# Kernel optimization log

Hardware: AMD Instinct MI355X
Metric: run time of the kernel (lower is better)

The kernel has to match this reference:

```python
import jax, jax.numpy as jnp
import numpy as np

B = 1_048_576
NUM_USERS = 6041
NUM_MOVIES = 3953
EMB_DIM = 32
NUM_GENRES = 18
HIDDEN = [64, 32, 16]
WIDE_DIM = NUM_USERS + NUM_MOVIES + 3 + NUM_GENRES  # gender, age, occupation scalars
DEEP_IN = 2 * EMB_DIM + 3 + NUM_GENRES              # = 85


def setup_inputs() -> dict:
    key = jax.random.key(0)
    ks = jax.random.split(key, 20)
    inp = {
        "user_ids": jax.random.randint(ks[0], (B,), 0, NUM_USERS),
        "movie_ids": jax.random.randint(ks[1], (B,), 0, NUM_MOVIES),
        "gender": jax.random.uniform(ks[2], (B,), dtype=jnp.float32),
        "age": jax.random.uniform(ks[3], (B,), dtype=jnp.float32),
        "occupation": jax.random.uniform(ks[4], (B,), dtype=jnp.float32),
        "genres": jax.random.uniform(ks[5], (B, NUM_GENRES), dtype=jnp.float32),
        # wide linear (out_features=1): weight vector + scalar bias
        "wide_W": jax.random.normal(ks[6], (WIDE_DIM,), dtype=jnp.float32) * 0.01,
        "wide_b": jnp.zeros((), dtype=jnp.float32),
        # embedding tables
        "user_table": jax.random.normal(ks[7], (NUM_USERS, EMB_DIM), dtype=jnp.float32) * 0.05,
        "movie_table": jax.random.normal(ks[8], (NUM_MOVIES, EMB_DIM), dtype=jnp.float32) * 0.05,
        # deep MLP params (stored as [in, out])
        "W1": jax.random.normal(ks[9], (DEEP_IN, HIDDEN[0]), dtype=jnp.float32) * 0.05,
        "b1": jnp.zeros((HIDDEN[0],), dtype=jnp.float32),
        "W2": jax.random.normal(ks[10], (HIDDEN[0], HIDDEN[1]), dtype=jnp.float32) * 0.05,
        "b2": jnp.zeros((HIDDEN[1],), dtype=jnp.float32),
        "W3": jax.random.normal(ks[11], (HIDDEN[1], HIDDEN[2]), dtype=jnp.float32) * 0.05,
        "b3": jnp.zeros((HIDDEN[2],), dtype=jnp.float32),
        "W4": jax.random.normal(ks[12], (HIDDEN[2], 1), dtype=jnp.float32) * 0.05,
        "b4": jnp.zeros((1,), dtype=jnp.float32),
    }
    return inp


def reference(user_ids, movie_ids, gender, age, occupation, genres,
              wide_W, wide_b, user_table, movie_table,
              W1, b1, W2, b2, W3, b3, W4, b4):
    nu = user_table.shape[0]
    nm = movie_table.shape[0]
    # dense (non-one-hot) part of the wide input: [B, 3 + num_genres]
    rest = jnp.concatenate(
        [gender[:, None], age[:, None], occupation[:, None], genres], axis=1)
    # one_hot @ W  ==  gather of the corresponding weight entries (same math,
    # without materializing the [B, nu+nm+21] one-hot matrix)
    w_user = wide_W[:nu]
    w_movie = wide_W[nu:nu + nm]
    w_rest = wide_W[nu + nm:]
    wide_out = w_user[user_ids] + w_movie[movie_ids] + rest @ w_rest + wide_b  # [B]

    # deep path (dropout is identity at inference)
    u_emb = user_table[user_ids]    # [B, 32]
    m_emb = movie_table[movie_ids]  # [B, 32]
    h = jnp.concatenate([u_emb, m_emb, rest], axis=1)  # [B, 85]
    h = jax.nn.relu(h @ W1 + b1)
    h = jax.nn.relu(h @ W2 + b2)
    h = jax.nn.relu(h @ W3 + b3)
    deep_out = (h @ W4 + b4)[:, 0]  # [B]

    return jax.nn.sigmoid(wide_out + deep_out)  # [B]
```

## Files before the change

kernel.cpp:

```cpp
#include <hip/hip_runtime.h>

#define NUSERS  6041
#define NMOVIES 3953
#define EMB     32
#define NGEN    18
#define H1N     64
#define H2N     32
#define H3N     16

typedef __bf16 bf16_t;
typedef bf16_t bf16x8 __attribute__((ext_vector_type(8)));
typedef float  f32x4  __attribute__((ext_vector_type(4)));
typedef float  f32x8  __attribute__((ext_vector_type(8)));

__device__ __forceinline__ f32x4 mfma16(bf16x8 a, bf16x8 b, f32x4 c) {
    return __builtin_amdgcn_mfma_f32_16x16x32_bf16(a, b, c, 0, 0, 0);
}
__device__ __forceinline__ bf16x8 cvt8(f32x8 v) {
    bf16x8 o;
    #pragma unroll
    for (int i = 0; i < 8; ++i) o[i] = (bf16_t)v[i];
    return o;
}

#define L1STRIDE 68
#define L2STRIDE 36
#define RSTRIDE  28
#define RBUFSZ   (16 * RSTRIDE)

struct Pref {
    float4 u0, u1, m0, m1;
    float  wu, wm;
};

__global__ __launch_bounds__(256)
void wd_fwd_pipe(const int*   __restrict__ user_ids,
                 const int*   __restrict__ movie_ids,
                 const float* __restrict__ gender,
                 const float* __restrict__ age,
                 const float* __restrict__ occupation,
                 const float* __restrict__ genres,
                 const float* __restrict__ wide_W,
                 const float* __restrict__ wide_b,
                 const float* __restrict__ user_table,
                 const float* __restrict__ movie_table,
                 const float* __restrict__ W1,
                 const float* __restrict__ b1,
                 const float* __restrict__ W2,
                 const float* __restrict__ b2,
                 const float* __restrict__ W3,
                 const float* __restrict__ b3,
                 const float* __restrict__ W4,
                 const float* __restrict__ b4,
                 float*       __restrict__ out,
                 int n)
{
    const int lane = threadIdx.x & 63;
    const int wib  = threadIdx.x >> 6;
    const int m    = lane & 15;
    const int quad = lane >> 4;

    __shared__ float lds_rest[4][2 * RBUFSZ];
    __shared__ float lds1[4][16 * L1STRIDE];
    __shared__ float lds2[4][16 * L2STRIDE];
    float* __restrict__ rbase = lds_rest[wib];
    float* __restrict__ L1p   = lds1[wib];
    float* __restrict__ L2p   = lds2[wib];

    for (int k = lane; k < 2 * RBUFSZ; k += 64) rbase[k] = 0.0f;

    bf16x8 B1f[3][4];
    #pragma unroll
    for (int kt = 0; kt < 3; ++kt)
        #pragma unroll
        for (int nt = 0; nt < 4; ++nt) {
            bf16x8 f;
            #pragma unroll
            for (int j = 0; j < 8; ++j) {
                const int k  = kt * 32 + quad * 8 + j;
                const float v = (k < 85) ? W1[k * H1N + nt * 16 + m] : 0.0f;
                f[j] = (bf16_t)v;
            }
            B1f[kt][nt] = f;
        }
    bf16x8 Bwf;
    {
        const float* wr = wide_W + NUSERS + NMOVIES;
        #pragma unroll
        for (int j = 0; j < 8; ++j) {
            const int k = 64 + quad * 8 + j;
            float v = 0.0f;
            if (m == 0) { if (k < 85) v = wr[k - 64]; else if (k == 85) v = 1.0f; }
            Bwf[j] = (bf16_t)v;
        }
    }
    bf16x8 B2f[2][2];
    #pragma unroll
    for (int kt = 0; kt < 2; ++kt)
        #pragma unroll
        for (int nt = 0; nt < 2; ++nt) {
            bf16x8 f;
            #pragma unroll
            for (int j = 0; j < 8; ++j)
                f[j] = (bf16_t)W2[(kt * 32 + quad * 8 + j) * H2N + nt * 16 + m];
            B2f[kt][nt] = f;
        }
    bf16x8 B3f;
    #pragma unroll
    for (int j = 0; j < 8; ++j) B3f[j] = (bf16_t)W3[(quad * 8 + j) * H3N + m];

    float bias1[4], bias2[2];
    #pragma unroll
    for (int nt = 0; nt < 4; ++nt) bias1[nt] = b1[nt * 16 + m];
    #pragma unroll
    for (int nt = 0; nt < 2; ++nt) bias2[nt] = b2[nt * 16 + m];
    const float bias3 = b3[m];
    const float w4v   = W4[m];
    const float b4v   = b4[0];
    const float wb0   = wide_b[0];

    const int ntiles = (n + 15) >> 4;
    const int gwave  = blockIdx.x * 4 + wib;
    const int nwaves = gridDim.x * 4;
    int niter = 0;
    if (gwave < ntiles) niter = (ntiles - gwave + nwaves - 1) / nwaves;
    const long gmax = (long)n * NGEN - 1;

#define LOAD_IDS(tt, U, M) { int rr = (tt) * 16 + m; rr = rr < n ? rr : n - 1; \
                             U = user_ids[rr]; M = movie_ids[rr]; }
#define LOAD_GENRES(tt, G, SC) { \
    const long gb = (long)(tt) * (16 * NGEN); \
    _Pragma("unroll") \
    for (int r = 0; r < 4; ++r) { long idx = gb + lane + r * 64; \
        idx = idx < gmax ? idx : gmax; G[r] = genres[idx]; } \
    { long idx = gb + lane + 256; idx = idx < gmax ? idx : gmax; \
      G[4] = (lane < 32) ? genres[idx] : 0.0f; } \
    { int rr = (tt) * 16 + m; rr = rr < n ? rr : n - 1; \
      const float* sp = (quad == 0) ? gender : (quad == 1) ? age : occupation; \
      SC = (quad < 3) ? sp[rr] : 0.0f; } }
#define WRITE_RBUF(B, G, SC) { \
    float* rb_ = rbase + (B) * RBUFSZ; \
    _Pragma("unroll") \
    for (int r = 0; r < 4; ++r) { int gi = lane + r * 64; int rw = gi / NGEN; \
        int cl = gi - rw * NGEN; rb_[rw * RSTRIDE + 3 + cl] = G[r]; } \
    if (lane < 32) { int gi = lane + 256; int rw = gi / NGEN; int cl = gi - rw * NGEN; \
        rb_[rw * RSTRIDE + 3 + cl] = G[4]; } \
    if (quad < 3) rb_[m * RSTRIDE + quad] = SC; }
#define ISSUE_GATHER(UID, MID, P) { \
    const float4* up_ = (const float4*)(user_table + (size_t)(UID) * EMB + quad * 8); \
    P.u0 = up_[0]; P.u1 = up_[1]; \
    const float4* mp_ = (const float4*)(movie_table + (size_t)(MID) * EMB + quad * 8); \
    P.m0 = mp_[0]; P.m1 = mp_[1]; \
    P.wu = wide_W[UID]; P.wm = wide_W[NUSERS + (MID)]; }

    if (niter > 0) {
        int t_c = gwave;
        int t_n = t_c + nwaves; if (t_n >= ntiles) t_n = t_c;

        int uid_c, mid_c, uid_n, mid_n, uid_n2, mid_n2;
        float gg_c[5], sc_c, gg_n[5], sc_n;
        Pref P_c, P_n;

        LOAD_IDS(t_c, uid_c, mid_c);
        LOAD_GENRES(t_c, gg_c, sc_c);
        ISSUE_GATHER(uid_c, mid_c, P_c);
        LOAD_IDS(t_n, uid_n, mid_n);
        WRITE_RBUF(0, gg_c, sc_c);
        uid_n2 = uid_n; mid_n2 = mid_n;
        int buf = 0;

        for (int i = 0; i < niter; ++i) {
            const float* rb = rbase + buf * RBUFSZ;
            const float4* sA = (const float4*)(rb + m * RSTRIDE + quad * 8);
            float4 a2a = sA[0], a2b = sA[1];

            const bool more = (i + 1 < niter);
            int t_n2 = t_n;
            if (more) {
                LOAD_GENRES(t_n, gg_n, sc_n);
                ISSUE_GATHER(uid_n, mid_n, P_n);
                t_n2 = t_n + nwaves; if (t_n2 >= ntiles) t_n2 = t_n;
                LOAD_IDS(t_n2, uid_n2, mid_n2);
            }

            const int base = t_c << 4;
            f32x8 vf;
            vf[0]=P_c.u0.x; vf[1]=P_c.u0.y; vf[2]=P_c.u0.z; vf[3]=P_c.u0.w;
            vf[4]=P_c.u1.x; vf[5]=P_c.u1.y; vf[6]=P_c.u1.z; vf[7]=P_c.u1.w;
            bf16x8 A0 = cvt8(vf);
            vf[0]=P_c.m0.x; vf[1]=P_c.m0.y; vf[2]=P_c.m0.z; vf[3]=P_c.m0.w;
            vf[4]=P_c.m1.x; vf[5]=P_c.m1.y; vf[6]=P_c.m1.z; vf[7]=P_c.m1.w;
            bf16x8 A1 = cvt8(vf);
            vf[0]=a2a.x; vf[1]=a2a.y; vf[2]=a2a.z; vf[3]=a2a.w;
            vf[4]=a2b.x; vf[5]=a2b.y; vf[6]=a2b.z; vf[7]=a2b.w;
            if (quad == 2) vf[5] = P_c.wu + P_c.wm + wb0;
            bf16x8 A2 = cvt8(vf);

            f32x4 accw = mfma16(A2, Bwf, (f32x4){0.f, 0.f, 0.f, 0.f});

            f32x4 acc[4];
            #pragma unroll
            for (int nt = 0; nt < 4; ++nt) {
                f32x4 c = {bias1[nt], bias1[nt], bias1[nt], bias1[nt]};
                c = mfma16(A0, B1f[0][nt], c);
                c = mfma16(A1, B1f[1][nt], c);
                c = mfma16(A2, B1f[2][nt], c);
                acc[nt] = c;
            }
            #pragma unroll
            for (int nt = 0; nt < 4; ++nt)
                #pragma unroll
                for (int r = 0; r < 4; ++r)
                    L1p[(quad * 4 + r) * L1STRIDE + nt * 16 + m] = fmaxf(acc[nt][r], 0.0f);

            bf16x8 AL2[2];
            #pragma unroll
            for (int kt = 0; kt < 2; ++kt) {
                const float4* s = (const float4*)(L1p + m * L1STRIDE + kt * 32 + quad * 8);
                float4 a = s[0], b = s[1];
                f32x8 t8; t8[0]=a.x; t8[1]=a.y; t8[2]=a.z; t8[3]=a.w;
                t8[4]=b.x; t8[5]=b.y; t8[6]=b.z; t8[7]=b.w;
                AL2[kt] = cvt8(t8);
            }

            f32x4 acc2[2];
            #pragma unroll
            for (int nt = 0; nt < 2; ++nt) {
                f32x4 c = {bias2[nt], bias2[nt], bias2[nt], bias2[nt]};
                c = mfma16(AL2[0], B2f[0][nt], c);
                c = mfma16(AL2[1], B2f[1][nt], c);
                acc2[nt] = c;
            }
            #pragma unroll
            for (int nt = 0; nt < 2; ++nt)
                #pragma unroll
                for (int r = 0; r < 4; ++r)
                    L2p[(quad * 4 + r) * L2STRIDE + nt * 16 + m] = fmaxf(acc2[nt][r], 0.0f);

            bf16x8 AL3;
            {
                const float4* s = (const float4*)(L2p + m * L2STRIDE + quad * 8);
                float4 a = s[0], b = s[1];
                f32x8 t8; t8[0]=a.x; t8[1]=a.y; t8[2]=a.z; t8[3]=a.w;
                t8[4]=b.x; t8[5]=b.y; t8[6]=b.z; t8[7]=b.w;
                AL3 = cvt8(t8);
            }

            f32x4 acc3 = mfma16(AL3, B3f, (f32x4){bias3, bias3, bias3, bias3});

            float t0 = fmaxf(acc3[0], 0.0f) * w4v + accw[0];
            float t1 = fmaxf(acc3[1], 0.0f) * w4v + accw[1];
            float t2 = fmaxf(acc3[2], 0.0f) * w4v + accw[2];
            float t3 = fmaxf(acc3[3], 0.0f) * w4v + accw[3];
            #pragma unroll
            for (int off = 1; off < 16; off <<= 1) {
                t0 += __shfl_xor(t0, off, 64);
                t1 += __shfl_xor(t1, off, 64);
                t2 += __shfl_xor(t2, off, 64);
                t3 += __shfl_xor(t3, off, 64);
            }
            if (m < 4) {
                float zv = t0;
                zv = (m == 1) ? t1 : zv;
                zv = (m == 2) ? t2 : zv;
                zv = (m == 3) ? t3 : zv;
                zv += b4v;
                const int orow = base + quad * 4 + m;
                if (orow < n) out[orow] = 1.0f / (1.0f + __expf(-zv));
            }

            if (more) {
                WRITE_RBUF(buf ^ 1, gg_n, sc_n);
                P_c = P_n;
                uid_c = uid_n; mid_c = mid_n;
                uid_n = uid_n2; mid_n = mid_n2;
                t_c = t_n; t_n = t_n2;
                buf ^= 1;
            }
        }
    }
#undef LOAD_IDS
#undef LOAD_GENRES
#undef WRITE_RBUF
#undef ISSUE_GATHER
}

extern "C" void kernel_launch(void* const* d_in, const int* in_sizes, int n_in,
                              void* d_out, int out_size, void* d_ws, size_t ws_size,
                              hipStream_t stream)
{
    const int*   user_ids   = (const int*)  d_in[0];
    const int*   movie_ids  = (const int*)  d_in[1];
    const float* gender     = (const float*)d_in[2];
    const float* age        = (const float*)d_in[3];
    const float* occupation = (const float*)d_in[4];
    const float* genres     = (const float*)d_in[5];
    const float* wide_W     = (const float*)d_in[6];
    const float* wide_b     = (const float*)d_in[7];
    const float* user_table = (const float*)d_in[8];
    const float* movie_table= (const float*)d_in[9];
    const float* W1         = (const float*)d_in[10];
    const float* b1         = (const float*)d_in[11];
    const float* W2         = (const float*)d_in[12];
    const float* b2         = (const float*)d_in[13];
    const float* W3         = (const float*)d_in[14];
    const float* b3         = (const float*)d_in[15];
    const float* W4         = (const float*)d_in[16];
    const float* b4         = (const float*)d_in[17];
    float*       out        = (float*)d_out;

    const int n = in_sizes[0];
    wd_fwd_pipe<<<1024, 256, 0, stream>>>(user_ids, movie_ids, gender, age, occupation,
                                          genres, wide_W, wide_b, user_table, movie_table,
                                          W1, b1, W2, b2, W3, b3, W4, b4, out, n);
}
```

Baseline: 216.2 us.

## Split into a bf16 prep pass and a leaner MFMA main kernel

Adds a prep kernel that converts both embedding tables and the per-row dense features (gender, age, occupation, genres) to bf16 in workspace, packing each row into 24 aligned bf16 values. The main kernel then loads MFMA A-fragments straight from these bf16 buffers, prefetches the next tile's ids and features, and folds the wide-path dot product into an extra MFMA. The goal is to cut conversion work and gather width inside the hot loop. The cost is an extra launch plus a write and re-read of the packed feature buffer. The old fused kernel remains as a fallback when workspace is missing or too small.

Result: slower. 241.3 us (+11.6%).

```diff
diff --git a/kernel.cpp b/kernel.cpp
--- a/kernel.cpp
+++ b/kernel.cpp
@@ -10,6 +10,7 @@
 
 typedef __bf16 bf16_t;
 typedef bf16_t bf16x8 __attribute__((ext_vector_type(8)));
+typedef bf16_t bf16x4 __attribute__((ext_vector_type(4)));
 typedef float  f32x4  __attribute__((ext_vector_type(4)));
 typedef float  f32x8  __attribute__((ext_vector_type(8)));
 
@@ -27,6 +28,269 @@
 #define L2STRIDE 36
 #define RSTRIDE  28
 #define RBUFSZ   (16 * RSTRIDE)
+
+#define RESTW 24
+
+#define TAB_U4   (NUSERS * EMB / 4)
+#define TAB_M4   (NMOVIES * EMB / 4)
+#define TAB4TOT  (TAB_U4 + TAB_M4)
+
+__global__ __launch_bounds__(256)
+void prep_all(const float* __restrict__ gender,
+              const float* __restrict__ age,
+              const float* __restrict__ occupation,
+              const float* __restrict__ genres,
+              const float* __restrict__ user_table,
+              const float* __restrict__ movie_table,
+              bf16_t* __restrict__ rest,
+              bf16_t* __restrict__ utab,
+              bf16_t* __restrict__ mtab,
+              int n)
+{
+    const int t = blockIdx.x * blockDim.x + threadIdx.x;
+
+    if (t < TAB4TOT) {
+        if (t < TAB_U4) {
+            float4 v = *(const float4*)(user_table + (size_t)t * 4);
+            bf16x4 o; o[0]=(bf16_t)v.x; o[1]=(bf16_t)v.y; o[2]=(bf16_t)v.z; o[3]=(bf16_t)v.w;
+            *(bf16x4*)(utab + (size_t)t * 4) = o;
+        } else {
+            const int u = t - TAB_U4;
+            float4 v = *(const float4*)(movie_table + (size_t)u * 4);
+            bf16x4 o; o[0]=(bf16_t)v.x; o[1]=(bf16_t)v.y; o[2]=(bf16_t)v.z; o[3]=(bf16_t)v.w;
+            *(bf16x4*)(mtab + (size_t)u * 4) = o;
+        }
+    }
+
+    if (t < n) {
+        const float* gr = genres + (size_t)t * NGEN;
+        float x[NGEN];
+        #pragma unroll
+        for (int j = 0; j < 9; ++j) {
+            float2 v = *(const float2*)(gr + 2 * j);
+            x[2 * j] = v.x; x[2 * j + 1] = v.y;
+        }
+        const float gg = gender[t], aa = age[t], oo = occupation[t];
+
+        bf16x8 c0, c1, c2;
+        c0[0]=(bf16_t)gg;  c0[1]=(bf16_t)aa;  c0[2]=(bf16_t)oo;
+        c0[3]=(bf16_t)x[0]; c0[4]=(bf16_t)x[1]; c0[5]=(bf16_t)x[2];
+        c0[6]=(bf16_t)x[3]; c0[7]=(bf16_t)x[4];
+        #pragma unroll
+        for (int j = 0; j < 8; ++j) c1[j] = (bf16_t)x[5 + j];
+        #pragma unroll
+        for (int j = 0; j < 5; ++j) c2[j] = (bf16_t)x[13 + j];
+        c2[5] = (bf16_t)0.0f; c2[6] = (bf16_t)0.0f; c2[7] = (bf16_t)0.0f;
+
+        bf16_t* op = rest + (size_t)t * RESTW;
+        *(bf16x8*)(op)      = c0;
+        *(bf16x8*)(op + 8)  = c1;
+        *(bf16x8*)(op + 16) = c2;
+    }
+}
+
+__global__ __launch_bounds__(256)
+void wd_fwd_main(const int*   __restrict__ user_ids,
+                 const int*   __restrict__ movie_ids,
+                 const float* __restrict__ wide_W,
+                 const float* __restrict__ wide_b,
+                 const float* __restrict__ W1,
+                 const float* __restrict__ b1,
+                 const float* __restrict__ W2,
+                 const float* __restrict__ b2,
+                 const float* __restrict__ W3,
+                 const float* __restrict__ b3,
+                 const float* __restrict__ W4,
+                 const float* __restrict__ b4,
+                 const bf16_t* __restrict__ utab,
+                 const bf16_t* __restrict__ mtab,
+                 const bf16_t* __restrict__ rest,
+                 float*       __restrict__ out,
+                 int n)
+{
+    const int lane = threadIdx.x & 63;
+    const int wib  = threadIdx.x >> 6;
+    const int m    = lane & 15;
+    const int quad = lane >> 4;
+
+    __shared__ float lds1[4][16 * L1STRIDE];
+    __shared__ float lds2[4][16 * L2STRIDE];
+    float* __restrict__ L1p = lds1[wib];
+    float* __restrict__ L2p = lds2[wib];
+
+    bf16x8 B1f[3][4];
+    #pragma unroll
+    for (int kt = 0; kt < 3; ++kt)
+        #pragma unroll
+        for (int nt = 0; nt < 4; ++nt) {
+            bf16x8 f;
+            #pragma unroll
+            for (int j = 0; j < 8; ++j) {
+                const int k  = kt * 32 + quad * 8 + j;
+                const float v = (k < 85) ? W1[k * H1N + nt * 16 + m] : 0.0f;
+                f[j] = (bf16_t)v;
+            }
+            B1f[kt][nt] = f;
+        }
+    bf16x8 Bwf;
+    {
+        const float* wr = wide_W + NUSERS + NMOVIES;
+        #pragma unroll
+        for (int j = 0; j < 8; ++j) {
+            const int k = 64 + quad * 8 + j;
+            float v = 0.0f;
+            if (m == 0) { if (k < 85) v = wr[k - 64]; else if (k == 85) v = 1.0f; }
+            Bwf[j] = (bf16_t)v;
+        }
+    }
+    bf16x8 B2f[2][2];
+    #pragma unroll
+    for (int kt = 0; kt < 2; ++kt)
+        #pragma unroll
+        for (int nt = 0; nt < 2; ++nt) {
+            bf16x8 f;
+            #pragma unroll
+            for (int j = 0; j < 8; ++j)
+                f[j] = (bf16_t)W2[(kt * 32 + quad * 8 + j) * H2N + nt * 16 + m];
+            B2f[kt][nt] = f;
+        }
+    bf16x8 B3f;
+    #pragma unroll
+    for (int j = 0; j < 8; ++j) B3f[j] = (bf16_t)W3[(quad * 8 + j) * H3N + m];
+
+    float bias1[4], bias2[2];
+    #pragma unroll
+    for (int nt = 0; nt < 4; ++nt) bias1[nt] = b1[nt * 16 + m];
+    #pragma unroll
+    for (int nt = 0; nt < 2; ++nt) bias2[nt] = b2[nt * 16 + m];
+    const float bias3 = b3[m];
+    const float w4v   = W4[m];
+    const float b4v   = b4[0];
+    const float wb0   = wide_b[0];
+
+    const int ntiles = (n + 15) >> 4;
+    const int gwave  = blockIdx.x * 4 + wib;
+    const int nwaves = gridDim.x * 4;
+    int niter = 0;
+    if (gwave < ntiles) niter = (ntiles - gwave + nwaves - 1) / nwaves;
+    if (niter == 0) return;
+
+    int t_c = gwave;
+    int t_n = t_c + nwaves; if (t_n >= ntiles) t_n = t_c;
+
+    int rc = t_c * 16 + m; if (rc >= n) rc = n - 1;
+    int uid_c = user_ids[rc], mid_c = movie_ids[rc];
+    bf16x8 A2c;
+    #pragma unroll
+    for (int j = 0; j < 8; ++j) A2c[j] = (bf16_t)0.0f;
+    if (quad < 3) A2c = *(const bf16x8*)(rest + (size_t)rc * RESTW + quad * 8);
+    float wuc = 0.0f, wmc = 0.0f;
+    if (quad == 2) { wuc = wide_W[uid_c]; wmc = wide_W[NUSERS + mid_c]; }
+
+    for (int i = 0; i < niter; ++i) {
+        const bf16x8 A0 = *(const bf16x8*)(utab + (size_t)uid_c * EMB + quad * 8);
+        const bf16x8 A1 = *(const bf16x8*)(mtab + (size_t)mid_c * EMB + quad * 8);
+
+        const bool more = (i + 1 < niter);
+        int uid_n = uid_c, mid_n = mid_c;
+        bf16x8 A2n = A2c;
+        float wun = wuc, wmn = wmc;
+        int t_n2 = t_n;
+        if (more) {
+            int rn = t_n * 16 + m; if (rn >= n) rn = n - 1;
+            uid_n = user_ids[rn]; mid_n = movie_ids[rn];
+            #pragma unroll
+            for (int j = 0; j < 8; ++j) A2n[j] = (bf16_t)0.0f;
+            if (quad < 3) A2n = *(const bf16x8*)(rest + (size_t)rn * RESTW + quad * 8);
+            wun = 0.0f; wmn = 0.0f;
+            if (quad == 2) { wun = wide_W[uid_n]; wmn = wide_W[NUSERS + mid_n]; }
+            t_n2 = t_n + nwaves; if (t_n2 >= ntiles) t_n2 = t_n;
+        }
+
+        const int base = t_c << 4;
+        bf16x8 A2 = A2c;
+        if (quad == 2) A2[5] = (bf16_t)(wuc + wmc + wb0);
+
+        f32x4 accw = mfma16(A2, Bwf, (f32x4){0.f, 0.f, 0.f, 0.f});
+
+        f32x4 acc[4];
+        #pragma unroll
+        for (int nt = 0; nt < 4; ++nt) {
+            f32x4 c = {bias1[nt], bias1[nt], bias1[nt], bias1[nt]};
+            c = mfma16(A2, B1f[2][nt], c);
+            c = mfma16(A1, B1f[1][nt], c);
+            c = mfma16(A0, B1f[0][nt], c);
+            acc[nt] = c;
+        }
+        #pragma unroll
+        for (int nt = 0; nt < 4; ++nt)
+            #pragma unroll
+            for (int r = 0; r < 4; ++r)
+                L1p[(quad * 4 + r) * L1STRIDE + nt * 16 + m] = fmaxf(acc[nt][r], 0.0f);
+
+        bf16x8 AL2[2];
+        #pragma unroll
+        for (int kt = 0; kt < 2; ++kt) {
+            const float4* s = (const float4*)(L1p + m * L1STRIDE + kt * 32 + quad * 8);
+            float4 a = s[0], b = s[1];
+            f32x8 t8; t8[0]=a.x; t8[1]=a.y; t8[2]=a.z; t8[3]=a.w;
+            t8[4]=b.x; t8[5]=b.y; t8[6]=b.z; t8[7]=b.w;
+            AL2[kt] = cvt8(t8);
+        }
+
+        f32x4 acc2[2];
+        #pragma unroll
+        for (int nt = 0; nt < 2; ++nt) {
+            f32x4 c = {bias2[nt], bias2[nt], bias2[nt], bias2[nt]};
+            c = mfma16(AL2[0], B2f[0][nt], c);
+            c = mfma16(AL2[1], B2f[1][nt], c);
+            acc2[nt] = c;
+        }
+        #pragma unroll
+        for (int nt = 0; nt < 2; ++nt)
+            #pragma unroll
+            for (int r = 0; r < 4; ++r)
+                L2p[(quad * 4 + r) * L2STRIDE + nt * 16 + m] = fmaxf(acc2[nt][r], 0.0f);
+
+        bf16x8 AL3;
+        {
+            const float4* s = (const float4*)(L2p + m * L2STRIDE + quad * 8);
+            float4 a = s[0], b = s[1];
+            f32x8 t8; t8[0]=a.x; t8[1]=a.y; t8[2]=a.z; t8[3]=a.w;
+            t8[4]=b.x; t8[5]=b.y; t8[6]=b.z; t8[7]=b.w;
+            AL3 = cvt8(t8);
+        }
+
+        f32x4 acc3 = mfma16(AL3, B3f, (f32x4){bias3, bias3, bias3, bias3});
+
+        float t0 = fmaxf(acc3[0], 0.0f) * w4v + accw[0];
+        float t1 = fmaxf(acc3[1], 0.0f) * w4v + accw[1];
+        float t2 = fmaxf(acc3[2], 0.0f) * w4v + accw[2];
+        float t3 = fmaxf(acc3[3], 0.0f) * w4v + accw[3];
+        #pragma unroll
+        for (int off = 1; off < 16; off <<= 1) {
+            t0 += __shfl_xor(t0, off, 64);
+            t1 += __shfl_xor(t1, off, 64);
+            t2 += __shfl_xor(t2, off, 64);
+            t3 += __shfl_xor(t3, off, 64);
+        }
+        if (m < 4) {
+            float zv = t0;
+            zv = (m == 1) ? t1 : zv;
+            zv = (m == 2) ? t2 : zv;
+            zv = (m == 3) ? t3 : zv;
+            zv += b4v;
+            const int orow = base + quad * 4 + m;
+            if (orow < n) out[orow] = 1.0f / (1.0f + __expf(-zv));
+        }
+
+        if (more) {
+            A2c = A2n; wuc = wun; wmc = wmn;
+            uid_c = uid_n; mid_c = mid_n;
+            t_c = t_n; t_n = t_n2;
+        }
+    }
+}
 
 struct Pref {
     float4 u0, u1, m0, m1;
@@ -310,7 +574,28 @@
     float*       out        = (float*)d_out;
 
     const int n = in_sizes[0];
-    wd_fwd_pipe<<<1024, 256, 0, stream>>>(user_ids, movie_ids, gender, age, occupation,
-                                          genres, wide_W, wide_b, user_table, movie_table,
-                                          W1, b1, W2, b2, W3, b3, W4, b4, out, n);
+
+    const size_t utab_bytes = ((size_t)NUSERS  * EMB * 2 + 255) & ~(size_t)255;
+    const size_t mtab_bytes = ((size_t)NMOVIES * EMB * 2 + 255) & ~(size_t)255;
+    const size_t rest_bytes = (size_t)n * RESTW * 2;
+    const size_t need = utab_bytes + mtab_bytes + rest_bytes;
+
+    if (d_ws != nullptr && ws_size >= need) {
+        bf16_t* utab = (bf16_t*)d_ws;
+        bf16_t* mtab = (bf16_t*)((char*)d_ws + utab_bytes);
+        bf16_t* rest = (bf16_t*)((char*)d_ws + utab_bytes + mtab_bytes);
+
+        const int prep_threads = (n > TAB4TOT) ? n : TAB4TOT;
+        const int prep_blocks  = (prep_threads + 255) / 256;
+        prep_all<<<prep_blocks, 256, 0, stream>>>(gender, age, occupation, genres,
+                                                  user_table, movie_table,
+                                                  rest, utab, mtab, n);
+        wd_fwd_main<<<1024, 256, 0, stream>>>(user_ids, movie_ids, wide_W, wide_b,
+                                              W1, b1, W2, b2, W3, b3, W4, b4,
+                                              utab, mtab, rest, out, n);
+    } else {
+        wd_fwd_pipe<<<1024, 256, 0, stream>>>(user_ids, movie_ids, gender, age, occupation,
+                                              genres, wide_W, wide_b, user_table, movie_table,
+                                              W1, b1, W2, b2, W3, b3, W4, b4, out, n);
+    }
 }
```

## Pre-pack embedding tables and MLP weights to bf16 in workspace before main kernel

Applied to the files above, without the earlier changes.

Adds a prep kernel that converts the user and movie embedding tables to bf16 and packs the W1/W2/W3 weights, b1, and the dense wide weights into MFMA fragment layout in workspace. A new main kernel loads these fragments straight into registers and gathers bf16 embedding rows, which halves gather bytes. It folds the wide-path dot product into an MFMA and uses a register-level software pipeline over 32-row tiles without LDS. The cost is an extra launch each call that re-converts the tables, and the main path runs only when workspace is large enough.

New measurement: 216.3 us. Within noise of the previous version (+0.0%).

```diff
diff --git a/kernel.cpp b/kernel.cpp
--- a/kernel.cpp
+++ b/kernel.cpp
@@ -10,6 +10,7 @@
 
 typedef __bf16 bf16_t;
 typedef bf16_t bf16x8 __attribute__((ext_vector_type(8)));
+typedef bf16_t bf16x4 __attribute__((ext_vector_type(4)));
 typedef float  f32x4  __attribute__((ext_vector_type(4)));
 typedef float  f32x8  __attribute__((ext_vector_type(8)));
 
@@ -27,6 +28,274 @@
 #define L2STRIDE 36
 #define RSTRIDE  28
 #define RBUFSZ   (16 * RSTRIDE)
+
+#define TAB_U4   (NUSERS * EMB / 4)
+#define TAB_M4   (NMOVIES * EMB / 4)
+#define TAB4TOT  (TAB_U4 + TAB_M4)
+#define TABBLOCKS ((TAB4TOT + 255) / 256)
+
+#define WPACK_HALF 9216
+#define WPACK_BYTES 18432
+
+__global__ __launch_bounds__(256)
+void prep_pack(const float* __restrict__ user_table,
+               const float* __restrict__ movie_table,
+               const float* __restrict__ W1,
+               const float* __restrict__ b1,
+               const float* __restrict__ W2,
+               const float* __restrict__ W3,
+               const float* __restrict__ wide_W,
+               bf16_t* __restrict__ utab,
+               bf16_t* __restrict__ mtab,
+               bf16_t* __restrict__ wpack)
+{
+    const int t = threadIdx.x;
+    const int b = blockIdx.x;
+
+    if (b < TABBLOCKS) {
+        const int u = b * 256 + t;
+        if (u < TAB4TOT) {
+            if (u < TAB_U4) {
+                float4 v = *(const float4*)(user_table + (size_t)u * 4);
+                bf16x4 o; o[0]=(bf16_t)v.x; o[1]=(bf16_t)v.y; o[2]=(bf16_t)v.z; o[3]=(bf16_t)v.w;
+                *(bf16x4*)(utab + (size_t)u * 4) = o;
+            } else {
+                const int w = u - TAB_U4;
+                float4 v = *(const float4*)(movie_table + (size_t)w * 4);
+                bf16x4 o; o[0]=(bf16_t)v.x; o[1]=(bf16_t)v.y; o[2]=(bf16_t)v.z; o[3]=(bf16_t)v.w;
+                *(bf16x4*)(mtab + (size_t)w * 4) = o;
+            }
+        }
+        return;
+    }
+
+    const int l  = t & 63;
+    const int f0 = t >> 6;
+    const int m  = l & 15;
+    const int q  = l >> 4;
+    const float* wr = wide_W + NUSERS + NMOVIES;
+
+    #pragma unroll
+    for (int p = 0; p < 5; ++p) {
+        const int f = f0 + p * 4;
+        if (f >= 18) break;
+        bf16x8 frag;
+        #pragma unroll
+        for (int j = 0; j < 8; ++j) {
+            float v = 0.0f;
+            if (f < 12) {
+                const int kt = f >> 2, nt = f & 3;
+                if (kt < 2) {
+                    v = W1[(kt * 32 + q * 8 + j) * H1N + nt * 16 + m];
+                } else if (q < 3) {
+                    if (j < 6)       v = W1[(67 + 6 * q + j) * H1N + nt * 16 + m];
+                    else if (q == 0) v = W1[(64 + (j - 6)) * H1N + nt * 16 + m];
+                    else if (q == 1) v = (j == 6) ? W1[66 * H1N + nt * 16 + m]
+                                                 : b1[nt * 16 + m];
+                }
+            } else if (f == 12) {
+                if (m == 0) {
+                    if (q < 3 && j < 6)        v = wr[3 + 6 * q + j];
+                    else if (q == 0)           v = wr[j - 6];
+                    else if (q == 1 && j == 6) v = wr[2];
+                    else if (q == 2 && j == 6) v = 1.0f;
+                }
+            } else if (f < 17) {
+                const int kt = (f - 13) >> 1, nt = (f - 13) & 1;
+                const int u = (2 * kt + (j >> 2)) * 16 + q * 4 + (j & 3);
+                v = W2[u * H2N + nt * 16 + m];
+            } else {
+                const int u = (j >> 2) * 16 + q * 4 + (j & 3);
+                v = W3[u * H3N + m];
+            }
+            frag[j] = (bf16_t)v;
+        }
+        *(bf16x8*)(wpack + ((size_t)f * 64 + l) * 8) = frag;
+    }
+}
+
+__global__ __launch_bounds__(256, 2)
+void wd_fwd_main2(const int*   __restrict__ user_ids,
+                  const int*   __restrict__ movie_ids,
+                  const float* __restrict__ gender,
+                  const float* __restrict__ age,
+                  const float* __restrict__ occupation,
+                  const float* __restrict__ genres,
+                  const float* __restrict__ wide_W,
+                  const float* __restrict__ wide_b,
+                  const float* __restrict__ b2,
+                  const float* __restrict__ b3,
+                  const float* __restrict__ W4,
+                  const float* __restrict__ b4,
+                  const bf16_t* __restrict__ utab,
+                  const bf16_t* __restrict__ mtab,
+                  const bf16_t* __restrict__ wpack,
+                  float*       __restrict__ out,
+                  int n)
+{
+    const int lane = threadIdx.x & 63;
+    const int m    = lane & 15;
+    const int quad = lane >> 4;
+
+    const bf16x8* wp = (const bf16x8*)wpack;
+    bf16x8 B1f[3][4];
+    #pragma unroll
+    for (int kt = 0; kt < 3; ++kt)
+        #pragma unroll
+        for (int nt = 0; nt < 4; ++nt)
+            B1f[kt][nt] = wp[(kt * 4 + nt) * 64 + lane];
+    const bf16x8 Bwf = wp[12 * 64 + lane];
+    bf16x8 B2f[2][2];
+    #pragma unroll
+    for (int kt = 0; kt < 2; ++kt)
+        #pragma unroll
+        for (int nt = 0; nt < 2; ++nt)
+            B2f[kt][nt] = wp[(13 + kt * 2 + nt) * 64 + lane];
+    const bf16x8 B3f = wp[17 * 64 + lane];
+
+    f32x4 bias2[2], bias3, w4f;
+    bias2[0] = *(const f32x4*)(b2 + quad * 4);
+    bias2[1] = *(const f32x4*)(b2 + 16 + quad * 4);
+    bias3    = *(const f32x4*)(b3 + quad * 4);
+    w4f      = *(const f32x4*)(W4 + quad * 4);
+    const float b4v = b4[0];
+    const float wb0 = wide_b[0];
+
+    const int nst   = (n + 31) >> 5;
+    const int gwave = (blockIdx.x * blockDim.x + threadIdx.x) >> 6;
+    const int nw    = (gridDim.x * blockDim.x) >> 6;
+    int niter = 0;
+    if (gwave < nst) niter = (nst - gwave + nw - 1) / nw;
+    if (niter == 0) return;
+
+    int st_c = gwave;
+    int st_n = st_c + nw; if (st_n >= nst) st_n = st_c;
+
+#define GATHER(row_, uid_, mid_, A0_, A1_, A2_) {                              \
+    A0_ = *(const bf16x8*)(utab + (size_t)(uid_) * EMB + quad * 8);            \
+    A1_ = *(const bf16x8*)(mtab + (size_t)(mid_) * EMB + quad * 8);            \
+    float2 g01 = {0.f,0.f}, g23 = {0.f,0.f}, g45 = {0.f,0.f};                  \
+    float s6 = 0.f, s7 = 0.f;                                                  \
+    if (quad < 3) {                                                            \
+        const float* gp_ = genres + (size_t)(row_) * NGEN + quad * 6;          \
+        g01 = *(const float2*)gp_;                                             \
+        g23 = *(const float2*)(gp_ + 2);                                       \
+        g45 = *(const float2*)(gp_ + 4);                                       \
+    }                                                                          \
+    if (quad == 0)      { s6 = gender[row_]; s7 = age[row_]; }                 \
+    else if (quad == 1) { s6 = occupation[row_]; s7 = 1.0f; }                  \
+    else if (quad == 2) { s6 = wide_W[uid_] + wide_W[NUSERS + (mid_)] + wb0; } \
+    A2_[0] = (bf16_t)g01.x; A2_[1] = (bf16_t)g01.y;                            \
+    A2_[2] = (bf16_t)g23.x; A2_[3] = (bf16_t)g23.y;                            \
+    A2_[4] = (bf16_t)g45.x; A2_[5] = (bf16_t)g45.y;                            \
+    A2_[6] = (bf16_t)s6;    A2_[7] = (bf16_t)s7; }
+
+    int ra = st_c * 32 + m;      if (ra >= n) ra = n - 1;
+    int rb = st_c * 32 + 16 + m; if (rb >= n) rb = n - 1;
+    int uidA = user_ids[ra], midA = movie_ids[ra];
+    int uidB = user_ids[rb], midB = movie_ids[rb];
+    bf16x8 A0a, A1a, A2a, A0b, A1b, A2b;
+    GATHER(ra, uidA, midA, A0a, A1a, A2a);
+    GATHER(rb, uidB, midB, A0b, A1b, A2b);
+    int ran = st_n * 32 + m;      if (ran >= n) ran = n - 1;
+    int rbn = st_n * 32 + 16 + m; if (rbn >= n) rbn = n - 1;
+    int uidAn = user_ids[ran], midAn = movie_ids[ran];
+    int uidBn = user_ids[rbn], midBn = movie_ids[rbn];
+
+    for (int i = 0; i < niter; ++i) {
+        const bool more = (i + 1 < niter);
+        bf16x8 A0an = A0a, A1an = A1a, A2an = A2a;
+        bf16x8 A0bn = A0b, A1bn = A1b, A2bn = A2b;
+        int uidA2 = uidAn, midA2 = midAn, uidB2 = uidBn, midB2 = midBn;
+        int st_n2 = st_n;
+        if (more) {
+            int ran_ = st_n * 32 + m;      if (ran_ >= n) ran_ = n - 1;
+            int rbn_ = st_n * 32 + 16 + m; if (rbn_ >= n) rbn_ = n - 1;
+            GATHER(ran_, uidAn, midAn, A0an, A1an, A2an);
+            GATHER(rbn_, uidBn, midBn, A0bn, A1bn, A2bn);
+            st_n2 = st_n + nw; if (st_n2 >= nst) st_n2 = st_n;
+            int ra2 = st_n2 * 32 + m;      if (ra2 >= n) ra2 = n - 1;
+            int rb2 = st_n2 * 32 + 16 + m; if (rb2 >= n) rb2 = n - 1;
+            uidA2 = user_ids[ra2]; midA2 = movie_ids[ra2];
+            uidB2 = user_ids[rb2]; midB2 = movie_ids[rb2];
+        }
+
+        const f32x4 z4 = {0.f, 0.f, 0.f, 0.f};
+        f32x4 accwA = mfma16(Bwf, A2a, z4);
+        f32x4 accwB = mfma16(Bwf, A2b, z4);
+
+        f32x4 aA[4], aB[4];
+        #pragma unroll
+        for (int nt = 0; nt < 4; ++nt) {
+            aA[nt] = mfma16(B1f[2][nt], A2a, z4);
+            aB[nt] = mfma16(B1f[2][nt], A2b, z4);
+        }
+        #pragma unroll
+        for (int nt = 0; nt < 4; ++nt) {
+            aA[nt] = mfma16(B1f[1][nt], A1a, aA[nt]);
+            aB[nt] = mfma16(B1f[1][nt], A1b, aB[nt]);
+        }
+        #pragma unroll
+        for (int nt = 0; nt < 4; ++nt) {
+            aA[nt] = mfma16(B1f[0][nt], A0a, aA[nt]);
+            aB[nt] = mfma16(B1f[0][nt], A0b, aB[nt]);
+        }
+
+        bf16x8 L2a[2], L2b[2];
+        #pragma unroll
+        for (int kt = 0; kt < 2; ++kt)
+            #pragma unroll
+            for (int r = 0; r < 4; ++r) {
+                L2a[kt][r]     = (bf16_t)fmaxf(aA[2 * kt][r],     0.f);
+                L2a[kt][4 + r] = (bf16_t)fmaxf(aA[2 * kt + 1][r], 0.f);
+                L2b[kt][r]     = (bf16_t)fmaxf(aB[2 * kt][r],     0.f);
+                L2b[kt][4 + r] = (bf16_t)fmaxf(aB[2 * kt + 1][r], 0.f);
+            }
+
+        f32x4 c2A[2], c2B[2];
+        #pragma unroll
+        for (int nt = 0; nt < 2; ++nt) {
+            c2A[nt] = mfma16(B2f[1][nt], L2a[1], mfma16(B2f[0][nt], L2a[0], bias2[nt]));
+            c2B[nt] = mfma16(B2f[1][nt], L2b[1], mfma16(B2f[0][nt], L2b[0], bias2[nt]));
+        }
+
+        bf16x8 L3a, L3b;
+        #pragma unroll
+        for (int r = 0; r < 4; ++r) {
+            L3a[r]     = (bf16_t)fmaxf(c2A[0][r], 0.f);
+            L3a[4 + r] = (bf16_t)fmaxf(c2A[1][r], 0.f);
+            L3b[r]     = (bf16_t)fmaxf(c2B[0][r], 0.f);
+            L3b[4 + r] = (bf16_t)fmaxf(c2B[1][r], 0.f);
+        }
+
+        f32x4 c3A = mfma16(B3f, L3a, bias3);
+        f32x4 c3B = mfma16(B3f, L3b, bias3);
+
+        float pA = fmaxf(c3A[0], 0.f) * w4f[0] + fmaxf(c3A[1], 0.f) * w4f[1]
+                 + fmaxf(c3A[2], 0.f) * w4f[2] + fmaxf(c3A[3], 0.f) * w4f[3];
+        float pB = fmaxf(c3B[0], 0.f) * w4f[0] + fmaxf(c3B[1], 0.f) * w4f[1]
+                 + fmaxf(c3B[2], 0.f) * w4f[2] + fmaxf(c3B[3], 0.f) * w4f[3];
+        pA += __shfl_xor(pA, 16, 64);  pA += __shfl_xor(pA, 32, 64);
+        pB += __shfl_xor(pB, 16, 64);  pB += __shfl_xor(pB, 32, 64);
+
+        if (lane < 16) {
+            const int base = st_c << 5;
+            const int oa = base + lane, ob = base + 16 + lane;
+            const float zA = pA + accwA[0] + b4v;
+            const float zB = pB + accwB[0] + b4v;
+            if (oa < n) out[oa] = 1.0f / (1.0f + __expf(-zA));
+            if (ob < n) out[ob] = 1.0f / (1.0f + __expf(-zB));
+        }
+
+        if (more) {
+            A0a = A0an; A1a = A1an; A2a = A2an;
+            A0b = A0bn; A1b = A1bn; A2b = A2bn;
+            uidAn = uidA2; midAn = midA2; uidBn = uidB2; midBn = midB2;
+            st_c = st_n; st_n = st_n2;
+        }
+    }
+#undef GATHER
+}
 
 struct Pref {
     float4 u0, u1, m0, m1;
@@ -310,7 +579,26 @@
     float*       out        = (float*)d_out;
 
     const int n = in_sizes[0];
-    wd_fwd_pipe<<<1024, 256, 0, stream>>>(user_ids, movie_ids, gender, age, occupation,
-                                          genres, wide_W, wide_b, user_table, movie_table,
-                                          W1, b1, W2, b2, W3, b3, W4, b4, out, n);
+
+    const size_t utab_bytes = ((size_t)NUSERS  * EMB * 2 + 255) & ~(size_t)255;
+    const size_t mtab_bytes = ((size_t)NMOVIES * EMB * 2 + 255) & ~(size_t)255;
+    const size_t need = utab_bytes + mtab_bytes + WPACK_BYTES;
+
+    if (d_ws != nullptr && ws_size >= need) {
+        bf16_t* utab  = (bf16_t*)d_ws;
+        bf16_t* mtab  = (bf16_t*)((char*)d_ws + utab_bytes);
+        bf16_t* wpack = (bf16_t*)((char*)d_ws + utab_bytes + mtab_bytes);
+
+        prep_pack<<<TABBLOCKS + 1, 256, 0, stream>>>(user_table, movie_table,
+                                                     W1, b1, W2, W3, wide_W,
+                                                     utab, mtab, wpack);
+        wd_fwd_main2<<<1024, 256, 0, stream>>>(user_ids, movie_ids,
+                                               gender, age, occupation, genres,
+                                               wide_W, wide_b, b2, b3, W4, b4,
+                                               utab, mtab, wpack, out, n);
+    } else {
+        wd_fwd_pipe<<<1024, 256, 0, stream>>>(user_ids, movie_ids, gender, age, occupation,
+                                              genres, wide_W, wide_b, user_table, movie_table,
+                                              W1, b1, W2, b2, W3, b3, W4, b4, out, n);
+    }
 }
```
